# Kernel optimization log

Measured on AMD Instinct MI355X. Metric: run time of the kernel, lower is better.

The kernel has to match this reference:

```python
import jax, jax.numpy as jnp
import numpy as np

K = 2        # kernel_size
DIL = 1      # dilation
H = 768      # h_size = nhid + nout
NOUT = 256
NLAYER = 10  # weight-tied iterations of f_theta


def conv1d(x, w, b, dilation=1):
    # x: (B, Cin, L), w: (Cout, Cin, K) -> (B, Cout, L-(K-1)*dilation)
    y = jax.lax.conv_general_dilated(
        x, w, window_strides=(1,), padding='VALID',
        rhs_dilation=(dilation,), dimension_numbers=('NCH', 'OIH', 'NCH'))
    return y + b[None, :, None]


def setup_inputs() -> dict:
    key = jax.random.key(0)
    ks = jax.random.split(key, 5)
    B, NINP, L = 4, 512, 1024
    bound = 0.01  # init_weights() uses N(0, 0.01)
    return {
        'X': jax.random.normal(ks[0], (B, NINP, L), dtype=jnp.float32),
        'z0': jnp.zeros((B, 2 * H, 1), dtype=jnp.float32),
        'inject_w': bound * jax.random.normal(ks[1], (4 * H, NINP, K), dtype=jnp.float32),
        'inject_b': bound * jax.random.normal(ks[2], (4 * H,), dtype=jnp.float32),
        'conv_w': bound * jax.random.normal(ks[3], (4 * H, H, K), dtype=jnp.float32),
        'conv_b': bound * jax.random.normal(ks[4], (4 * H,), dtype=jnp.float32),
    }


def reference(X, z0, inject_w, inject_b, conv_w, conv_b):
    B, _, L = X.shape
    pad_in = K - 1            # inject conv causal padding
    pad_h = (K - 1) * DIL     # hidden conv causal padding

    # us = inject_conv(pad(X)) : (B, 4H, L), computed once
    Xp = jnp.pad(X, ((0, 0), (0, 0), (pad_in, 0)))
    us = conv1d(Xp, inject_w, inject_b, dilation=1)

    z0h, z0c = z0[:, :H], z0[:, H:]  # (B, H, 1) each
    hid_pad = jnp.broadcast_to(z0h, (B, H, pad_h))  # repeat history into padding

    def step(z1s, _):
        z1h, z1c = z1s[:, :H], z1s[:, H:]
        # shifted cell state: cat([z0c, z1c])[:, :, :-1]
        z0c_s = jnp.concatenate([z0c, z1c[:, :, :-1]], axis=2)
        # weight-tied causal dilated conv on hidden part, history in padding
        xh = jnp.concatenate([hid_pad, z1h], axis=2)
        out = us + conv1d(xh, conv_w, conv_b, dilation=DIL)  # (B, 4H, L)
        it, ot, gt, ft = jnp.split(out, 4, axis=1)
        ct = jax.nn.sigmoid(ft) * z0c_s + jax.nn.sigmoid(it) * jnp.tanh(gt)
        ht = jax.nn.sigmoid(ot) * jnp.tanh(ct)
        return jnp.concatenate([ht, ct], axis=1), None

    z1s0 = jnp.zeros((B, 2 * H, L), dtype=X.dtype)
    z1s, _ = jax.lax.scan(step, z1s0, None, length=NLAYER)

    out = jnp.transpose(z1s[:, H - NOUT:H], (0, 2, 1))  # (B, L, nout)
    z0_out = z1s[:, :, -1:]                              # history repackaging
    return out, z0_out
```

## Files before the change

kernel.cpp:

```cpp
#include <hip/hip_runtime.h>
#include <hip/hip_bf16.h>
#include <stdint.h>


#define B_    4
#define L_    1024
#define LP1   1025
#define H_    768
#define NG_   3072
#define NINP_ 512
#define NOUT_ 256

typedef __bf16 bf16x8 __attribute__((ext_vector_type(8)));
typedef float f32x4 __attribute__((ext_vector_type(4)));
typedef _Float16 f16x4 __attribute__((ext_vector_type(4)));
using bf16_t = __hip_bfloat16;

__device__ __forceinline__ float sigf(float x){ return 1.f/(1.f + __expf(-x)); }
__device__ __forceinline__ float tanhf_(float x){
  float e = __expf(-2.f*fabsf(x));
  float r = (1.f - e)/(1.f + e);
  return x >= 0.f ? r : -r;
}

__device__ __forceinline__ void gl_lds16(const void* g, void* l){
  __builtin_amdgcn_global_load_lds(
    (const __attribute__((address_space(1))) uint32_t*)g,
    (__attribute__((address_space(3))) uint32_t*)l, 16, 0, 0);
}

__global__ void init_k(const float* __restrict__ z0, bf16_t* __restrict__ Xt,
                       bf16_t* __restrict__ Hb0, bf16_t* __restrict__ Hb1,
                       _Float16* __restrict__ Cb0, _Float16* __restrict__ Cb1){
  int tid = blockIdx.x*256 + threadIdx.x;
  if (tid < B_*NINP_){
    int b = tid >> 9, i = tid & 511;
    Xt[(size_t)b*LP1*NINP_ + i] = __float2bfloat16(0.f);
  }
  if (tid < B_*H_){
    int b = tid / H_, j = tid % H_;
    size_t idx = (size_t)b*LP1*H_ + j;
    bf16_t hz = __float2bfloat16(z0[b*2*H_ + j]);
    _Float16 cz = (_Float16)z0[b*2*H_ + H_ + j];
    Hb0[idx] = hz; Hb1[idx] = hz; Cb0[idx] = cz; Cb1[idx] = cz;
  }
}

__global__ void prep_w(const float* __restrict__ iw, const float* __restrict__ ib,
                       const float* __restrict__ cw, const float* __restrict__ cb,
                       bf16_t* __restrict__ Wit, bf16_t* __restrict__ Wct,
                       float* __restrict__ bias4){
  int op = blockIdx.x;
  int gate = (op >> 4) & 3;
  int j = ((op >> 6) << 4) | (op & 15);
  int o = gate*H_ + j;
  const float2* s2 = (const float2*)(iw + (size_t)o*NINP_*2);
  bf16_t* d = Wit + (size_t)op*(2*NINP_);
  for (int i = threadIdx.x; i < NINP_; i += 256){
    float2 v = s2[i];
    d[i]         = __float2bfloat16(v.x);
    d[NINP_ + i] = __float2bfloat16(v.y);
  }
  const float2* c2 = (const float2*)(cw + (size_t)o*H_*2);
  bf16_t* dc = Wct + (size_t)op*(2*H_);
  for (int i = threadIdx.x; i < H_; i += 256){
    float2 v = c2[i];
    dc[i]      = __float2bfloat16(v.x);
    dc[H_ + i] = __float2bfloat16(v.y);
  }
  if (threadIdx.x == 0) bias4[j*4 + gate] = ib[o] + cb[o];
}

__global__ void transpose_x(const float* __restrict__ X, bf16_t* __restrict__ Xt){
  __shared__ float tile[64][65];
  int b = blockIdx.z;
  int t0 = blockIdx.x*64, i0 = blockIdx.y*64;
  int c = threadIdx.x & 63;
  for (int r = threadIdx.x >> 6; r < 64; r += 4)
    tile[r][c] = X[((size_t)b*NINP_ + i0 + r)*L_ + t0 + c];
  __syncthreads();
  for (int r = threadIdx.x >> 6; r < 64; r += 4)
    Xt[((size_t)b*LP1 + t0 + r + 1)*NINP_ + i0 + c] = __float2bfloat16(tile[c][r]);
}

template<int KTOT, int AROW, int MODE>
__launch_bounds__(256, 3)
__global__ void gemmF(const bf16_t* __restrict__ A, const bf16_t* __restrict__ Bt,
                      const float* __restrict__ bias4, f16x4* __restrict__ us4,
                      const _Float16* __restrict__ Cprev, _Float16* __restrict__ Cnew,
                      bf16_t* __restrict__ Hnew, float* __restrict__ outF, int bn_base){
  __shared__ __align__(1024) char smem[49152];

  const int tid = threadIdx.x;
  const int l  = tid & 63;
  const int w  = tid >> 6;
  const int wm = w >> 1, wn = w & 1;
  const int lr = l & 15;
  const int lk = l >> 4;

  const int nwg = gridDim.x * gridDim.y;
  int flat = blockIdx.y * gridDim.x + blockIdx.x;
  flat = (flat & 7) * (nwg >> 3) + (flat >> 3);
  const int bm0 = (flat & 31) * 128;
  const int bn0 = bn_base + (flat >> 5) * 128;

  f32x4 acc[4][4];
#pragma unroll
  for (int i = 0; i < 4; ++i)
#pragma unroll
    for (int jj = 0; jj < 4; ++jj)
      acc[i][jj] = (f32x4){0.f,0.f,0.f,0.f};

  const int rg = l >> 2;
  const int cg = (l & 3) ^ (rg & 3);
  const char* ag[2]; const char* bg[2];
#pragma unroll
  for (int n = 0; n < 2; ++n){
    const int mf = w*2 + n;
    const int m = bm0 + mf*16 + rg;
    const int b = m >> 10, t = m & 1023;
    ag[n] = (const char*)A + (size_t)(b*LP1 + t)*(AROW*2) + cg*16;
    const int nc = bn0 + mf*16 + rg;
    bg[n] = (const char*)Bt + (size_t)nc*(KTOT*2) + cg*16;
  }
  const int a0off = (w*2    )*1024;
  const int a1off = (w*2 + 1)*1024;

  const int rdoff = lr*64 + ((lk ^ (lr & 3)) << 4);

#define STAGE_AT(S, KO) { \
    char* base_ = smem + (S)*16384; \
    gl_lds16(ag[0] + (KO), base_ + a0off); \
    gl_lds16(ag[1] + (KO), base_ + a1off); \
    gl_lds16(bg[0] + (KO), base_ + 8192 + a0off); \
    gl_lds16(bg[1] + (KO), base_ + 8192 + a1off); }

#define COMPUTE_AT(S) { \
    const char* sp_ = smem + (S)*16384 + rdoff; \
    bf16x8 af[4], bv[4]; \
    _Pragma("unroll") for (int f = 0; f < 4; ++f) \
      af[f] = *(const bf16x8*)(sp_ + (wm*4 + f)*1024); \
    _Pragma("unroll") for (int f = 0; f < 4; ++f) \
      bv[f] = *(const bf16x8*)(sp_ + 8192 + (wn*4 + f)*1024); \
    __builtin_amdgcn_s_setprio(1); \
    _Pragma("unroll") for (int fm = 0; fm < 4; ++fm) \
      _Pragma("unroll") for (int fn = 0; fn < 4; ++fn) \
        acc[fm][fn] = __builtin_amdgcn_mfma_f32_16x16x32_bf16(af[fm], bv[fn], acc[fm][fn], 0, 0, 0); \
    __builtin_amdgcn_s_setprio(0); }

  constexpr int NT = KTOT / 32;

  STAGE_AT(0, 0)
  STAGE_AT(1, 64)
  int slot = 0;
  for (int t = 0; t < NT; ++t){
    if (t < NT - 1) { asm volatile("s_waitcnt vmcnt(4)" ::: "memory"); }
    else            { asm volatile("s_waitcnt vmcnt(0)" ::: "memory"); }
    __builtin_amdgcn_s_barrier();
    if (t + 2 < NT){
      const int s2 = (slot >= 1) ? slot - 1 : 2;
      STAGE_AT(s2, (t + 2) << 6)
    }
    COMPUTE_AT(slot)
    slot = (slot < 2) ? slot + 1 : 0;
  }

#undef STAGE_AT
#undef COMPUTE_AT

  const int jblk = (bn0 >> 6) + wn;
  const int j = jblk*16 + lr;
  const int rq = lk << 2;

  if (MODE == 0){
    const float4 bz = ((const float4*)bias4)[j];
#pragma unroll
    for (int fm = 0; fm < 4; ++fm){
      const int mbase = bm0 + wm*64 + fm*16 + rq;
#pragma unroll
      for (int r = 0; r < 4; ++r){
        const int m = mbase + r;
        const int b = m >> 10, t = m & 1023;
        const float ig = acc[fm][0][r] + bz.x;
        const float og = acc[fm][1][r] + bz.y;
        const float gg = acc[fm][2][r] + bz.z;
        const float fg = acc[fm][3][r] + bz.w;
        us4[(size_t)m*H_ + j] = (f16x4){ (_Float16)ig, (_Float16)og,
                                         (_Float16)gg, (_Float16)fg };
        const float cp = (t == 0) ? (float)Cprev[(size_t)b*LP1*H_ + j] : 0.f;
        const float c  = sigf(fg)*cp + sigf(ig)*tanhf_(gg);
        const float h  = sigf(og)*tanhf_(c);
        const size_t hcb = (size_t)(b*LP1 + t)*H_ + j;
        Cnew[hcb + H_] = (_Float16)c;
        Hnew[hcb + H_] = __float2bfloat16(h);
      }
    }
  } else {
    f16x4 uv[4][4]; _Float16 cp16[4][4];
#pragma unroll
    for (int fm = 0; fm < 4; ++fm){
      const int mbase = bm0 + wm*64 + fm*16 + rq;
#pragma unroll
      for (int r = 0; r < 4; ++r){
        const int m = mbase + r;
        const int b = m >> 10, t = m & 1023;
        uv[fm][r]  = us4[(size_t)m*H_ + j];
        cp16[fm][r] = Cprev[(size_t)(b*LP1 + t)*H_ + j];
      }
    }
#pragma unroll
    for (int fm = 0; fm < 4; ++fm){
      const int mbase = bm0 + wm*64 + fm*16 + rq;
#pragma unroll
      for (int r = 0; r < 4; ++r){
        const int m = mbase + r;
        const int b = m >> 10, t = m & 1023;
        const float ig = acc[fm][0][r] + (float)uv[fm][r][0];
        const float og = acc[fm][1][r] + (float)uv[fm][r][1];
        const float gg = acc[fm][2][r] + (float)uv[fm][r][2];
        const float fg = acc[fm][3][r] + (float)uv[fm][r][3];
        const float c  = sigf(fg)*(float)cp16[fm][r] + sigf(ig)*tanhf_(gg);
        const float h  = sigf(og)*tanhf_(c);
        if (MODE == 1){
          const size_t hcb = (size_t)(b*LP1 + t)*H_ + j;
          Cnew[hcb + H_] = (_Float16)c;
          Hnew[hcb + H_] = __float2bfloat16(h);
        } else {
          outF[(size_t)(b*1024 + t)*NOUT_ + (j - (H_ - NOUT_))] = h;
        }
      }
    }
  }
}

__global__ void tail_k(const bf16_t* __restrict__ H8, const _Float16* __restrict__ C8,
                       const f16x4* __restrict__ us4, const bf16_t* __restrict__ Wct,
                       float* __restrict__ out){
  const int b = blockIdx.y;
  const int op = blockIdx.x*256 + threadIdx.x;
  const int gate = (op >> 4) & 3, lr = op & 15;
  const int j = ((op >> 6) << 4) | lr;
  const bf16_t* a  = H8 + (size_t)(b*LP1 + 1023)*H_;
  const bf16_t* wr = Wct + (size_t)op*1536;
  float s = 0.f;
#pragma unroll 4
  for (int k2 = 0; k2 < 1536; k2 += 8){
    bf16x8 av = *reinterpret_cast<const bf16x8*>(a + k2);
    bf16x8 wv = *reinterpret_cast<const bf16x8*>(wr + k2);
#pragma unroll
    for (int u = 0; u < 8; ++u) s += (float)av[u]*(float)wv[u];
  }
  s += (float)us4[(size_t)(b*1024 + 1023)*H_ + j][gate];
  const float si = __shfl(s, lr);
  const float so = __shfl(s, lr + 16);
  const float sg = __shfl(s, lr + 32);
  const float sf = __shfl(s, lr + 48);
  if (gate == 0){
    const float cp = (float)C8[(size_t)(b*LP1 + 1023)*H_ + j];
    const float c = sigf(sf)*cp + sigf(si)*tanhf_(sg);
    const float h = sigf(so)*tanhf_(c);
    out[B_*L_*NOUT_ + b*2*H_ + j]      = h;
    out[B_*L_*NOUT_ + b*2*H_ + H_ + j] = c;
  }
}

extern "C" void kernel_launch(void* const* d_in, const int* in_sizes, int n_in,
                              void* d_out, int out_size, void* d_ws, size_t ws_size,
                              hipStream_t stream){
  const float* X   = (const float*)d_in[0];
  const float* z0  = (const float*)d_in[1];
  const float* iw  = (const float*)d_in[2];
  const float* ib  = (const float*)d_in[3];
  const float* cw  = (const float*)d_in[4];
  const float* cbv = (const float*)d_in[5];
  float* out = (float*)d_out;

  char* ws = (char*)d_ws;
  f16x4*    us4  = (f16x4*)   (ws + 0);
  bf16_t*   Xt   = (bf16_t*)  (ws + 25165824);
  bf16_t*   Wit  = (bf16_t*)  (ws + 29364224);
  bf16_t*   Wct  = (bf16_t*)  (ws + 35655680);
  float*    bias4= (float*)   (ws + 45092864);
  bf16_t*   Hb0  = (bf16_t*)  (ws + 45105152);
  bf16_t*   Hb1  = (bf16_t*)  (ws + 51402752);
  _Float16* Cb0  = (_Float16*)(ws + 57700352);
  _Float16* Cb1  = (_Float16*)(ws + 63997952);

  init_k<<<12, 256, 0, stream>>>(z0, Xt, Hb0, Hb1, Cb0, Cb1);
  prep_w<<<NG_, 256, 0, stream>>>(iw, ib, cw, cbv, Wit, Wct, bias4);
  transpose_x<<<dim3(L_/64, NINP_/64, B_), 256, 0, stream>>>(X, Xt);

  gemmF<1024, NINP_, 0><<<dim3(32, 24), 256, 0, stream>>>(
      Xt, Wit, bias4, us4, Cb0, Cb0, Hb0, nullptr, 0);

  bf16_t* Hp = Hb0; _Float16* Cp = Cb0;
  bf16_t* Hn = Hb1; _Float16* Cn = Cb1;
  for (int it = 1; it <= 8; ++it){
    gemmF<1536, H_, 1><<<dim3(32, 24), 256, 0, stream>>>(
        Hp, Wct, nullptr, us4, Cp, Cn, Hn, nullptr, 0);
    bf16_t* th = Hp; Hp = Hn; Hn = th;
    _Float16* tc = Cp; Cp = Cn; Cn = tc;
  }

  tail_k<<<dim3(12, B_), 256, 0, stream>>>(Hp, Cp, us4, Wct, out);

  gemmF<1536, H_, 2><<<dim3(32, 8), 256, 0, stream>>>(
      Hp, Wct, nullptr, us4, Cp, nullptr, nullptr, out, 2048);
}
```

Before: 634.0 us.

## Store activations and weights in pre-tiled MFMA fragment layout with duplicated shifted copies

Activations (X, hidden state) and weights are now written in a blocked 16x32 tile layout that matches the MFMA fragment order. The causal shift is handled by keeping two copies of each activation buffer: the current step and the step shifted by one. This lets each wave load one contiguous 1 KB chunk per tile, with no swizzle or row-strided gathers, and removes the padded transpose. The cost is writing two H copies per step, with scattered 2-byte stores in the epilogue, plus extra workspace.

Result: faster. 609.7 us (-3.8%).

```diff
diff --git a/kernel.cpp b/kernel.cpp
--- a/kernel.cpp
+++ b/kernel.cpp
@@ -29,66 +29,77 @@
     (__attribute__((address_space(3))) uint32_t*)l, 16, 0, 0);
 }
 
-__global__ void init_k(const float* __restrict__ z0, bf16_t* __restrict__ Xt,
-                       bf16_t* __restrict__ Hb0, bf16_t* __restrict__ Hb1,
-                       _Float16* __restrict__ Cb0, _Float16* __restrict__ Cb1){
+__device__ __forceinline__ size_t htile_idx(int b, int t, int j){
+  return ((size_t)((b*64 + (t>>4))*24) + (j>>5))*512
+         + (size_t)((t&15)*8 + ((j>>3)&3)*128 + (j&7));
+}
+
+__global__ void init_k(const float* __restrict__ z0, bf16_t* __restrict__ XB,
+                       bf16_t* __restrict__ HB0, bf16_t* __restrict__ HB1,
+                       _Float16* __restrict__ C0, _Float16* __restrict__ C1){
   int tid = blockIdx.x*256 + threadIdx.x;
   if (tid < B_*NINP_){
-    int b = tid >> 9, i = tid & 511;
-    Xt[(size_t)b*LP1*NINP_ + i] = __float2bfloat16(0.f);
+    int b = tid >> 9, r = tid & 511;
+    int kb = r>>5, lk = (r>>3)&3, e = r&7;
+    XB[((size_t)(b*64*16) + kb)*512 + lk*128 + e] = __float2bfloat16(0.f);
   }
   if (tid < B_*H_){
     int b = tid / H_, j = tid % H_;
-    size_t idx = (size_t)b*LP1*H_ + j;
     bf16_t hz = __float2bfloat16(z0[b*2*H_ + j]);
     _Float16 cz = (_Float16)z0[b*2*H_ + H_ + j];
-    Hb0[idx] = hz; Hb1[idx] = hz; Cb0[idx] = cz; Cb1[idx] = cz;
+    size_t a = ((size_t)(b*64*24) + (j>>5))*512 + ((j>>3)&3)*128 + (j&7);
+    HB0[a] = hz; HB1[a] = hz;
+    size_t idx = (size_t)b*LP1*H_ + j;
+    C0[idx] = cz; C1[idx] = cz;
   }
 }
 
 __global__ void prep_w(const float* __restrict__ iw, const float* __restrict__ ib,
                        const float* __restrict__ cw, const float* __restrict__ cb,
-                       bf16_t* __restrict__ Wit, bf16_t* __restrict__ Wct,
+                       bf16_t* __restrict__ WitT, bf16_t* __restrict__ WctT,
                        float* __restrict__ bias4){
   int op = blockIdx.x;
   int gate = (op >> 4) & 3;
   int j = ((op >> 6) << 4) | (op & 15);
   int o = gate*H_ + j;
+  int nt = op >> 4, lrow = op & 15;
   const float2* s2 = (const float2*)(iw + (size_t)o*NINP_*2);
-  bf16_t* d = Wit + (size_t)op*(2*NINP_);
   for (int i = threadIdx.x; i < NINP_; i += 256){
     float2 v = s2[i];
-    d[i]         = __float2bfloat16(v.x);
-    d[NINP_ + i] = __float2bfloat16(v.y);
+    int k0 = i, k1 = NINP_ + i;
+    WitT[((size_t)(nt*32 + (k0>>5)))*512 + lrow*8 + ((k0>>3)&3)*128 + (k0&7)] = __float2bfloat16(v.x);
+    WitT[((size_t)(nt*32 + (k1>>5)))*512 + lrow*8 + ((k1>>3)&3)*128 + (k1&7)] = __float2bfloat16(v.y);
   }
   const float2* c2 = (const float2*)(cw + (size_t)o*H_*2);
-  bf16_t* dc = Wct + (size_t)op*(2*H_);
   for (int i = threadIdx.x; i < H_; i += 256){
     float2 v = c2[i];
-    dc[i]      = __float2bfloat16(v.x);
-    dc[H_ + i] = __float2bfloat16(v.y);
+    int k0 = i, k1 = H_ + i;
+    WctT[((size_t)(nt*48 + (k0>>5)))*512 + lrow*8 + ((k0>>3)&3)*128 + (k0&7)] = __float2bfloat16(v.x);
+    WctT[((size_t)(nt*48 + (k1>>5)))*512 + lrow*8 + ((k1>>3)&3)*128 + (k1&7)] = __float2bfloat16(v.y);
   }
   if (threadIdx.x == 0) bias4[j*4 + gate] = ib[o] + cb[o];
 }
 
-__global__ void transpose_x(const float* __restrict__ X, bf16_t* __restrict__ Xt){
-  __shared__ float tile[64][65];
-  int b = blockIdx.z;
-  int t0 = blockIdx.x*64, i0 = blockIdx.y*64;
-  int c = threadIdx.x & 63;
-  for (int r = threadIdx.x >> 6; r < 64; r += 4)
-    tile[r][c] = X[((size_t)b*NINP_ + i0 + r)*L_ + t0 + c];
-  __syncthreads();
-  for (int r = threadIdx.x >> 6; r < 64; r += 4)
-    Xt[((size_t)b*LP1 + t0 + r + 1)*NINP_ + i0 + c] = __float2bfloat16(tile[c][r]);
-}
-
-template<int KTOT, int AROW, int MODE>
+__global__ void tile_x(const float* __restrict__ X, bf16_t* __restrict__ XA,
+                       bf16_t* __restrict__ XB){
+  int b = blockIdx.z, i = blockIdx.y;
+  int t = blockIdx.x*256 + threadIdx.x;
+  bf16_t bv = __float2bfloat16(X[((size_t)b*NINP_ + i)*L_ + t]);
+  int kb = i>>5, lk = (i>>3)&3, e = i&7;
+  XA[((size_t)((b*64 + (t>>4))*16) + kb)*512 + (t&15)*8 + lk*128 + e] = bv;
+  if (t < L_-1){
+    int t1 = t + 1;
+    XB[((size_t)((b*64 + (t1>>4))*16) + kb)*512 + (t1&15)*8 + lk*128 + e] = bv;
+  }
+}
+
+template<int KTOT, int MODE>
 __launch_bounds__(256, 3)
-__global__ void gemmF(const bf16_t* __restrict__ A, const bf16_t* __restrict__ Bt,
-                      const float* __restrict__ bias4, f16x4* __restrict__ us4,
-                      const _Float16* __restrict__ Cprev, _Float16* __restrict__ Cnew,
-                      bf16_t* __restrict__ Hnew, float* __restrict__ outF, int bn_base){
+__global__ void gemmF(const bf16_t* __restrict__ A1, const bf16_t* __restrict__ A0,
+                      const bf16_t* __restrict__ Bt, const float* __restrict__ bias4,
+                      f16x4* __restrict__ us4, const _Float16* __restrict__ Cprev,
+                      _Float16* __restrict__ Cnew, bf16_t* __restrict__ HAn,
+                      bf16_t* __restrict__ HBn, float* __restrict__ outF, int bn_base){
   __shared__ __align__(1024) char smem[49152];
 
   const int tid = threadIdx.x;
@@ -111,32 +122,36 @@
     for (int jj = 0; jj < 4; ++jj)
       acc[i][jj] = (f32x4){0.f,0.f,0.f,0.f};
 
-  const int rg = l >> 2;
-  const int cg = (l & 3) ^ (rg & 3);
-  const char* ag[2]; const char* bg[2];
+  constexpr int KB0 = (KTOT == 1024) ? 16 : 24;
+  constexpr int KBB = KTOT / 32;
+  const int bI = bm0 >> 10;
+  const int g0 = (bm0 >> 4) & 63;
+
+  const char* a0p[2]; const char* a1p[2]; const char* bp[2];
 #pragma unroll
   for (int n = 0; n < 2; ++n){
-    const int mf = w*2 + n;
-    const int m = bm0 + mf*16 + rg;
-    const int b = m >> 10, t = m & 1023;
-    ag[n] = (const char*)A + (size_t)(b*LP1 + t)*(AROW*2) + cg*16;
-    const int nc = bn0 + mf*16 + rg;
-    bg[n] = (const char*)Bt + (size_t)nc*(KTOT*2) + cg*16;
+    const int g = g0 + w*2 + n;
+    a0p[n] = (const char*)A0 + (((size_t)(bI*64 + g)*KB0) << 10) + l*16;
+    a1p[n] = (const char*)A1 + (((size_t)(bI*64 + g)*KB0) << 10) + l*16;
+    const int nt = (bn0 >> 4) + w*2 + n;
+    bp[n]  = (const char*)Bt + (((size_t)nt*KBB) << 10) + l*16;
   }
   const int a0off = (w*2    )*1024;
   const int a1off = (w*2 + 1)*1024;
 
-  const int rdoff = lr*64 + ((lk ^ (lr & 3)) << 4);
-
-#define STAGE_AT(S, KO) { \
+#define STAGE_AT(S, T) { \
     char* base_ = smem + (S)*16384; \
-    gl_lds16(ag[0] + (KO), base_ + a0off); \
-    gl_lds16(ag[1] + (KO), base_ + a1off); \
-    gl_lds16(bg[0] + (KO), base_ + 8192 + a0off); \
-    gl_lds16(bg[1] + (KO), base_ + 8192 + a1off); }
+    const int T_ = (T); \
+    const size_t koA = (size_t)(T_ < KB0 ? T_ : T_ - KB0) << 10; \
+    const char* as0 = (T_ < KB0) ? a0p[0] : a1p[0]; \
+    const char* as1 = (T_ < KB0) ? a0p[1] : a1p[1]; \
+    gl_lds16(as0 + koA, base_ + a0off); \
+    gl_lds16(as1 + koA, base_ + a1off); \
+    gl_lds16(bp[0] + ((size_t)T_ << 10), base_ + 8192 + a0off); \
+    gl_lds16(bp[1] + ((size_t)T_ << 10), base_ + 8192 + a1off); }
 
 #define COMPUTE_AT(S) { \
-    const char* sp_ = smem + (S)*16384 + rdoff; \
+    const char* sp_ = smem + (S)*16384 + l*16; \
     bf16x8 af[4], bv[4]; \
     _Pragma("unroll") for (int f = 0; f < 4; ++f) \
       af[f] = *(const bf16x8*)(sp_ + (wm*4 + f)*1024); \
@@ -151,7 +166,7 @@
   constexpr int NT = KTOT / 32;
 
   STAGE_AT(0, 0)
-  STAGE_AT(1, 64)
+  STAGE_AT(1, 1)
   int slot = 0;
   for (int t = 0; t < NT; ++t){
     if (t < NT - 1) { asm volatile("s_waitcnt vmcnt(4)" ::: "memory"); }
@@ -159,7 +174,7 @@
     __builtin_amdgcn_s_barrier();
     if (t + 2 < NT){
       const int s2 = (slot >= 1) ? slot - 1 : 2;
-      STAGE_AT(s2, (t + 2) << 6)
+      STAGE_AT(s2, t + 2)
     }
     COMPUTE_AT(slot)
     slot = (slot < 2) ? slot + 1 : 0;
@@ -190,9 +205,10 @@
         const float cp = (t == 0) ? (float)Cprev[(size_t)b*LP1*H_ + j] : 0.f;
         const float c  = sigf(fg)*cp + sigf(ig)*tanhf_(gg);
         const float h  = sigf(og)*tanhf_(c);
-        const size_t hcb = (size_t)(b*LP1 + t)*H_ + j;
-        Cnew[hcb + H_] = (_Float16)c;
-        Hnew[hcb + H_] = __float2bfloat16(h);
+        Cnew[(size_t)(b*LP1 + t + 1)*H_ + j] = (_Float16)c;
+        bf16_t hb = __float2bfloat16(h);
+        HAn[htile_idx(b, t, j)] = hb;
+        if (t < L_-1) HBn[htile_idx(b, t+1, j)] = hb;
       }
     }
   } else {
@@ -204,7 +220,7 @@
       for (int r = 0; r < 4; ++r){
         const int m = mbase + r;
         const int b = m >> 10, t = m & 1023;
-        uv[fm][r]  = us4[(size_t)m*H_ + j];
+        uv[fm][r]   = us4[(size_t)m*H_ + j];
         cp16[fm][r] = Cprev[(size_t)(b*LP1 + t)*H_ + j];
       }
     }
@@ -222,9 +238,10 @@
         const float c  = sigf(fg)*(float)cp16[fm][r] + sigf(ig)*tanhf_(gg);
         const float h  = sigf(og)*tanhf_(c);
         if (MODE == 1){
-          const size_t hcb = (size_t)(b*LP1 + t)*H_ + j;
-          Cnew[hcb + H_] = (_Float16)c;
-          Hnew[hcb + H_] = __float2bfloat16(h);
+          Cnew[(size_t)(b*LP1 + t + 1)*H_ + j] = (_Float16)c;
+          bf16_t hb = __float2bfloat16(h);
+          HAn[htile_idx(b, t, j)] = hb;
+          if (t < L_-1) HBn[htile_idx(b, t+1, j)] = hb;
         } else {
           outF[(size_t)(b*1024 + t)*NOUT_ + (j - (H_ - NOUT_))] = h;
         }
@@ -233,22 +250,27 @@
   }
 }
 
-__global__ void tail_k(const bf16_t* __restrict__ H8, const _Float16* __restrict__ C8,
-                       const f16x4* __restrict__ us4, const bf16_t* __restrict__ Wct,
-                       float* __restrict__ out){
+__global__ void tail_k(const bf16_t* __restrict__ HA9, const bf16_t* __restrict__ HB9,
+                       const _Float16* __restrict__ C9, const f16x4* __restrict__ us4,
+                       const bf16_t* __restrict__ WctT, float* __restrict__ out){
   const int b = blockIdx.y;
   const int op = blockIdx.x*256 + threadIdx.x;
   const int gate = (op >> 4) & 3, lr = op & 15;
   const int j = ((op >> 6) << 4) | lr;
-  const bf16_t* a  = H8 + (size_t)(b*LP1 + 1023)*H_;
-  const bf16_t* wr = Wct + (size_t)op*1536;
+  const int nt = op >> 4;
   float s = 0.f;
+  const size_t gbase = (size_t)(b*64 + 63) * 24;
 #pragma unroll 4
-  for (int k2 = 0; k2 < 1536; k2 += 8){
-    bf16x8 av = *reinterpret_cast<const bf16x8*>(a + k2);
-    bf16x8 wv = *reinterpret_cast<const bf16x8*>(wr + k2);
-#pragma unroll
-    for (int u = 0; u < 8; ++u) s += (float)av[u]*(float)wv[u];
+  for (int kb = 0; kb < 48; ++kb){
+    const bf16_t* hsrc = (kb < 24) ? HB9 + (gbase + kb)*512
+                                   : HA9 + (gbase + (kb - 24))*512;
+#pragma unroll
+    for (int lkk = 0; lkk < 4; ++lkk){
+      bf16x8 av = *reinterpret_cast<const bf16x8*>(hsrc + 120 + lkk*128);
+      bf16x8 wv = *reinterpret_cast<const bf16x8*>(WctT + ((size_t)(nt*48 + kb))*512 + lr*8 + lkk*128);
+#pragma unroll
+      for (int u = 0; u < 8; ++u) s += (float)av[u]*(float)wv[u];
+    }
   }
   s += (float)us4[(size_t)(b*1024 + 1023)*H_ + j][gate];
   const float si = __shfl(s, lr);
@@ -256,7 +278,7 @@
   const float sg = __shfl(s, lr + 32);
   const float sf = __shfl(s, lr + 48);
   if (gate == 0){
-    const float cp = (float)C8[(size_t)(b*LP1 + 1023)*H_ + j];
+    const float cp = (float)C9[(size_t)(b*LP1 + 1023)*H_ + j];
     const float c = sigf(sf)*cp + sigf(si)*tanhf_(sg);
     const float h = sigf(so)*tanhf_(c);
     out[B_*L_*NOUT_ + b*2*H_ + j]      = h;
@@ -277,33 +299,37 @@
 
   char* ws = (char*)d_ws;
   f16x4*    us4  = (f16x4*)   (ws + 0);
-  bf16_t*   Xt   = (bf16_t*)  (ws + 25165824);
-  bf16_t*   Wit  = (bf16_t*)  (ws + 29364224);
-  bf16_t*   Wct  = (bf16_t*)  (ws + 35655680);
-  float*    bias4= (float*)   (ws + 45092864);
-  bf16_t*   Hb0  = (bf16_t*)  (ws + 45105152);
-  bf16_t*   Hb1  = (bf16_t*)  (ws + 51402752);
-  _Float16* Cb0  = (_Float16*)(ws + 57700352);
-  _Float16* Cb1  = (_Float16*)(ws + 63997952);
-
-  init_k<<<12, 256, 0, stream>>>(z0, Xt, Hb0, Hb1, Cb0, Cb1);
-  prep_w<<<NG_, 256, 0, stream>>>(iw, ib, cw, cbv, Wit, Wct, bias4);
-  transpose_x<<<dim3(L_/64, NINP_/64, B_), 256, 0, stream>>>(X, Xt);
-
-  gemmF<1024, NINP_, 0><<<dim3(32, 24), 256, 0, stream>>>(
-      Xt, Wit, bias4, us4, Cb0, Cb0, Hb0, nullptr, 0);
-
-  bf16_t* Hp = Hb0; _Float16* Cp = Cb0;
-  bf16_t* Hn = Hb1; _Float16* Cn = Cb1;
+  bf16_t*   XA   = (bf16_t*)  (ws + 25165824);
+  bf16_t*   XB   = (bf16_t*)  (ws + 29360128);
+  bf16_t*   WitT = (bf16_t*)  (ws + 33554432);
+  bf16_t*   WctT = (bf16_t*)  (ws + 39845888);
+  float*    bias4= (float*)   (ws + 49283072);
+  bf16_t*   HA0  = (bf16_t*)  (ws + 49295360);
+  bf16_t*   HB0  = (bf16_t*)  (ws + 55586816);
+  bf16_t*   HA1  = (bf16_t*)  (ws + 61878272);
+  bf16_t*   HB1  = (bf16_t*)  (ws + 68169728);
+  _Float16* C0   = (_Float16*)(ws + 74461184);
+  _Float16* C1   = (_Float16*)(ws + 80758784);
+
+  init_k<<<12, 256, 0, stream>>>(z0, XB, HB0, HB1, C0, C1);
+  prep_w<<<NG_, 256, 0, stream>>>(iw, ib, cw, cbv, WitT, WctT, bias4);
+  tile_x<<<dim3(4, NINP_, B_), 256, 0, stream>>>(X, XA, XB);
+
+  gemmF<1024, 0><<<dim3(32, 24), 256, 0, stream>>>(
+      XA, XB, WitT, bias4, us4, C0, C0, HA0, HB0, nullptr, 0);
+
+  bf16_t* HAp = HA0; bf16_t* HBp = HB0; _Float16* Cp = C0;
+  bf16_t* HAn = HA1; bf16_t* HBn = HB1; _Float16* Cn = C1;
   for (int it = 1; it <= 8; ++it){
-    gemmF<1536, H_, 1><<<dim3(32, 24), 256, 0, stream>>>(
-        Hp, Wct, nullptr, us4, Cp, Cn, Hn, nullptr, 0);
-    bf16_t* th = Hp; Hp = Hn; Hn = th;
+    gemmF<1536, 1><<<dim3(32, 24), 256, 0, stream>>>(
+        HAp, HBp, WctT, nullptr, us4, Cp, Cn, HAn, HBn, nullptr, 0);
+    bf16_t* ta = HAp; HAp = HAn; HAn = ta;
+    bf16_t* tb = HBp; HBp = HBn; HBn = tb;
     _Float16* tc = Cp; Cp = Cn; Cn = tc;
   }
 
-  tail_k<<<dim3(12, B_), 256, 0, stream>>>(Hp, Cp, us4, Wct, out);
-
-  gemmF<1536, H_, 2><<<dim3(32, 8), 256, 0, stream>>>(
-      Hp, Wct, nullptr, us4, Cp, nullptr, nullptr, out, 2048);
-}
+  tail_k<<<dim3(12, B_), 256, 0, stream>>>(HAp, HBp, Cp, us4, WctT, out);
+
+  gemmF<1536, 2><<<dim3(32, 8), 256, 0, stream>>>(
+      HAp, HBp, WctT, nullptr, us4, Cp, nullptr, nullptr, nullptr, out, 2048);
+}
```
